# Optimization experiments

Hardware: AMD Instinct MI355X
Metric: run time of the kernel (lower is better)

The kernel has to match this reference:

```python
import jax, jax.numpy as jnp
import numpy as np

B, T, D, N = 64, 32, 128, 128


def setup_inputs() -> dict:
    key = jax.random.key(0)
    ks = jax.random.split(key, 7)
    init_mu = 0.05
    ini_sigma = -4.6
    inp = {
        'x': jax.random.normal(ks[0], (B, T, D), dtype=jnp.float32),
        'U_z': init_mu * jax.random.normal(ks[1], (D, N), dtype=jnp.float32),
        'W_z': init_mu * jax.random.normal(ks[2], (N, N), dtype=jnp.float32),
        'U_r': init_mu * jax.random.normal(ks[3], (D, N), dtype=jnp.float32),
        'W_r': init_mu * jax.random.normal(ks[4], (N, N), dtype=jnp.float32),
        'U_h': init_mu * jax.random.normal(ks[5], (D, N), dtype=jnp.float32),
        'W_h': init_mu * jax.random.normal(ks[6], (N, N), dtype=jnp.float32),
        'uz_sigma': jnp.full((N,), ini_sigma, dtype=jnp.float32),
        'wz_sigma': jnp.full((N,), ini_sigma, dtype=jnp.float32),
        'ur_sigma': jnp.full((N,), ini_sigma, dtype=jnp.float32),
        'wr_sigma': jnp.full((N,), ini_sigma, dtype=jnp.float32),
        'uh_sigma': jnp.full((N,), ini_sigma, dtype=jnp.float32),
        'wh_sigma': jnp.full((N,), ini_sigma, dtype=jnp.float32),
    }
    return inp


def _outer(a, b):
    # [B,n] x [B,n] -> [B,n,n]
    return a[:, :, None] * b[:, None, :]


def _hadamard_sigma(s1, s2, m1, m2):
    # s1*s2 + diag(m1) s2 diag(m1) + diag(m2) s1 diag(m2)
    return s1 * s2 + _outer(m1, m1) * s2 + _outer(m2, m2) * s1


def reference(x, U_z, W_z, U_r, W_r, U_h, W_h,
              uz_sigma, wz_sigma, ur_sigma, wr_sigma, uh_sigma, wh_sigma):
    b, t, d = x.shape
    n = U_z.shape[1]
    idx = jnp.arange(n)
    sp = jax.nn.softplus
    dUz, dWz = jnp.diag(sp(uz_sigma)), jnp.diag(sp(wz_sigma))
    dUr, dWr = jnp.diag(sp(ur_sigma)), jnp.diag(sp(wr_sigma))
    dUh, dWh = jnp.diag(sp(uh_sigma)), jnp.diag(sp(wh_sigma))

    def step(carry, xt):
        mu_p, S_p = carry  # [B,n], [B,n,n]
        xx = jnp.sum(xt * xt, axis=1)[:, None, None]
        pp = jnp.sum(mu_p * mu_p, axis=1)[:, None, None]
        trS = jnp.trace(S_p, axis1=1, axis2=2)[:, None, None]

        def gate_cov(W, dW, dU):
            # W^T Sigma W + ||prev||^2 dW + tr(Sigma) dW + ||x||^2 dU
            S1 = jnp.einsum('ki,bkl,lj->bij', W, S_p, W)
            return S1 + pp * dW + trS * dW + xx * dU

        az = xt @ U_z + mu_p @ W_z
        z = jax.nn.sigmoid(az)
        gz = z * (1.0 - z)
        S_z = gate_cov(W_z, dWz, dUz) * _outer(gz, gz)

        ar = xt @ U_r + mu_p @ W_r
        r = jax.nn.sigmoid(ar)
        gr = r * (1.0 - r)
        S_r = gate_cov(W_r, dWr, dUr) * _outer(gr, gr)

        rh = mu_p * r
        ah = xt @ U_h + rh @ W_h
        h = jnp.tanh(ah)
        gh = 1.0 - h * h
        S_g = _hadamard_sigma(S_p, S_r, mu_p, r)
        rr = jnp.sum(rh * rh, axis=1)[:, None, None]
        trg = jnp.trace(S_g, axis1=1, axis2=2)[:, None, None]
        S_hh = jnp.einsum('ki,bkl,lj->bij', W_h, S_g, W_h) + rr * dWh + trg * dWh + xx * dUh
        S_h = S_hh * _outer(gh, gh)

        mu = z * mu_p + (1.0 - z) * h
        sa = _hadamard_sigma(S_z, S_p, z, mu_p)
        sb = _hadamard_sigma(S_z, S_h, 1.0 - z, h)
        S = sa + sb - S_z * _outer(mu_p, h) - S_z * _outer(h, mu_p)
        S = jnp.where(jnp.isfinite(S), S, jnp.zeros_like(S))
        S = S.at[:, idx, idx].set(jnp.abs(S[:, idx, idx]))
        return (mu, S), (mu, S)

    mu0 = jnp.zeros((b, n), dtype=x.dtype)
    S0 = jnp.zeros((b, n, n), dtype=x.dtype)
    _, (mu_seq, S_seq) = jax.lax.scan(step, (mu0, S0), jnp.swapaxes(x, 0, 1))
    # [B,T,n], [B,T,n,n]
    return jnp.swapaxes(mu_seq, 0, 1), jnp.swapaxes(S_seq, 0, 1)
```

## Files before the change

kernel.cpp:

```cpp
#include <hip/hip_runtime.h>
#include <math.h>

#define B_ 64
#define T_ 32
#define D_ 128
#define N_ 128
#define SBS 72
#define PTS 136

typedef __attribute__((ext_vector_type(8))) short s8v;
typedef __attribute__((ext_vector_type(4))) float f4;

__device__ __forceinline__ float softplus_f(float v){ return (v > 20.f) ? v : log1pf(expf(v)); }
__device__ __forceinline__ float sigmoid_f(float v){ return 1.f / (1.f + expf(-v)); }
__device__ __forceinline__ float wred(float v){
#pragma unroll
    for (int o = 32; o > 0; o >>= 1) v += __shfl_down(v, o, 64);
    return v;
}
__device__ __forceinline__ void split2(float v, unsigned short& h, unsigned short& l){
    unsigned int u  = __float_as_uint(v);
    unsigned int rh = u + 0x7fffu + ((u >> 16) & 1u);
    h = (unsigned short)(rh >> 16);
    float fh = __uint_as_float(rh & 0xffff0000u);
    float lo = v - fh;
    unsigned int ul = __float_as_uint(lo);
    unsigned int rl = ul + 0x7fffu + ((ul >> 16) & 1u);
    l = (unsigned short)(rl >> 16);
}
__device__ __forceinline__ void split4_store(float4 v, unsigned short* hp, unsigned short* lp){
    unsigned short h0,h1,h2,h3,l0,l1,l2,l3;
    split2(v.x,h0,l0); split2(v.y,h1,l1); split2(v.z,h2,l2); split2(v.w,h3,l3);
    uint2 H = make_uint2((unsigned)h0 | ((unsigned)h1 << 16), (unsigned)h2 | ((unsigned)h3 << 16));
    uint2 L = make_uint2((unsigned)l0 | ((unsigned)l1 << 16), (unsigned)l2 | ((unsigned)l3 << 16));
    *(uint2*)hp = H; *(uint2*)lp = L;
}
__device__ __forceinline__ f4 mfma3(s8v ah, s8v al, s8v bh, s8v bl, f4 c){
    c = __builtin_amdgcn_mfma_f32_16x16x32_bf16(ah, bh, c, 0, 0, 0);
    c = __builtin_amdgcn_mfma_f32_16x16x32_bf16(ah, bl, c, 0, 0, 0);
    c = __builtin_amdgcn_mfma_f32_16x16x32_bf16(al, bh, c, 0, 0, 0);
    return c;
}

__global__ __launch_bounds__(256)
void prep_w(const float* __restrict__ Wz, const float* __restrict__ Wr,
            const float* __restrict__ Wh, unsigned short* __restrict__ WT){
    int gate = blockIdx.x, n0 = blockIdx.y * 16, tid = threadIdx.x;
    const float* W = (gate == 0) ? Wz : (gate == 1) ? Wr : Wh;
    unsigned short* hi = WT + (size_t)gate * 32768;
    unsigned short* lo = hi + 16384;
#pragma unroll
    for (int e = 0; e < 8; ++e){
        int idx = tid + e * 256;
        int n = n0 + (idx >> 7), k = idx & 127;
        float v = W[(size_t)k * 128 + n];
        unsigned short h, l; split2(v, h, l);
        hi[(size_t)n * 128 + k] = h;
        lo[(size_t)n * 128 + k] = l;
    }
}

__global__ __launch_bounds__(256)
void prep_xu(const float* __restrict__ x, const float* __restrict__ Uz,
             const float* __restrict__ Ur, const float* __restrict__ Uh,
             float* __restrict__ XU, float* __restrict__ XX){
    int bt = blockIdx.x, tid = threadIdx.x;
    __shared__ float sX[128];
    __shared__ float sRed[256];
    __shared__ float sP[4];
    if (tid < 128) sX[tid] = x[(size_t)bt * 128 + tid];
    __syncthreads();
    {
        float v = (tid < 128) ? sX[tid] * sX[tid] : 0.f;
        v = wred(v);
        if ((tid & 63) == 0) sP[tid >> 6] = v;
    }
    const float* Us[3] = {Uz, Ur, Uh};
#pragma unroll 1
    for (int g = 0; g < 3; ++g){
        int n = tid & 127, hf = tid >> 7;
        float p = 0.f;
#pragma unroll 8
        for (int k = hf * 64; k < hf * 64 + 64; ++k) p = fmaf(sX[k], Us[g][(size_t)k * 128 + n], p);
        sRed[tid] = p;
        __syncthreads();
        if (tid < 128) XU[(size_t)g * (2048 * 128) + (size_t)bt * 128 + tid] = sRed[tid] + sRed[tid + 128];
        __syncthreads();
    }
    if (tid == 0) XX[bt] = sP[0] + sP[1] + sP[2] + sP[3];
}

__global__ __launch_bounds__(256, 1)
void step_zr(const float* __restrict__ Wz, const float* __restrict__ Wr, const float* __restrict__ Wh,
             const float* __restrict__ uzs, const float* __restrict__ wzs,
             const float* __restrict__ urs, const float* __restrict__ wrs,
             const unsigned short* __restrict__ WT,
             const float* __restrict__ XU, const float* __restrict__ XX,
             float* __restrict__ mu_out, const float* __restrict__ S_out,
             float* __restrict__ wsSz, float* __restrict__ wsSr,
             float* __restrict__ wsVec, int t)
{
    const int b = blockIdx.y, j0 = blockIdx.x * 32, tid = threadIdx.x;
    const int lane = tid & 63, w = tid >> 6, q = (tid >> 4) & 3, lm = tid & 15;

    __shared__ alignas(16) char sBig[36864];
    unsigned short* sShi = (unsigned short*)sBig;
    unsigned short* sSlo = (unsigned short*)(sBig + 128 * SBS * 2);
    unsigned short* sPT  = (unsigned short*)sBig;

    __shared__ float sMu[128], sZ[128], sGz[128], sR[128], sGr[128], sRh[128];
    __shared__ float sSP[4][128];
    __shared__ float sRed[256];
    __shared__ float sScalA[4], sScalB[4], sScalC[4];

    const int bt = b * T_ + t;
    const float* Sp = (t > 0) ? (S_out + (size_t)(bt - 1) * 16384) : S_out;

    if (tid < 128) sMu[tid] = (t > 0) ? mu_out[(size_t)(bt - 1) * 128 + tid] : 0.f;
    for (int a = tid; a < 512; a += 256){
        int tb = a >> 7, n = a & 127;
        const float* src = (tb == 0) ? uzs : (tb == 1) ? wzs : (tb == 2) ? urs : wrs;
        sSP[tb][n] = softplus_f(src[n]);
    }
    __syncthreads();

    {
        int g = tid >> 7, n = tid & 127;
        const float* Wg = g ? Wr : Wz;
        float a = XU[(size_t)g * (2048 * 128) + (size_t)bt * 128 + n];
#pragma unroll 16
        for (int k = 0; k < 128; ++k) a = fmaf(sMu[k], Wg[(size_t)k * 128 + n], a);
        float gg = sigmoid_f(a);
        if (!g){ sZ[n] = gg; sGz[n] = gg * (1.f - gg); }
        else   { sR[n] = gg; sGr[n] = gg * (1.f - gg); }
    }
    __syncthreads();

    if (tid < 128) sRh[tid] = sMu[tid] * sR[tid];
    {
        float v1 = (tid < 128) ? sMu[tid] * sMu[tid] : 0.f;
        float v2 = (tid < 128 && t > 0) ? Sp[(size_t)tid * 129] : 0.f;
        v1 = wred(v1); v2 = wred(v2);
        if (lane == 0){ sScalA[w] = v1; sScalB[w] = v2; }
    }
    __syncthreads();

    {
        int n = tid & 127, hf = tid >> 7;
        float p = 0.f;
#pragma unroll 16
        for (int k = hf * 64; k < hf * 64 + 64; ++k) p = fmaf(sRh[k], Wh[(size_t)k * 128 + n], p);
        sRed[tid] = p;
        float v = (tid < 128) ? sRh[tid] * sRh[tid] : 0.f;
        v = wred(v);
        if (lane == 0) sScalC[w] = v;
    }
    __syncthreads();

    if (tid < 128){
        float ah = XU[(size_t)2 * (2048 * 128) + (size_t)bt * 128 + tid] + sRed[tid] + sRed[tid + 128];
        float h = tanhf(ah);
        float z = sZ[tid];
        if (blockIdx.x == 0){
            mu_out[(size_t)bt * 128 + tid] = z * sMu[tid] + (1.f - z) * h;
            float* vbp = wsVec + (size_t)b * 520;
            vbp[tid] = z; vbp[128 + tid] = sR[tid]; vbp[256 + tid] = h; vbp[384 + tid] = 1.f - h * h;
            if (tid == 0) vbp[512] = sScalC[0] + sScalC[1] + sScalC[2] + sScalC[3];
        }
    }

    f4 accP[8];
#pragma unroll
    for (int i = 0; i < 8; ++i) accP[i] = (f4){0.f, 0.f, 0.f, 0.f};

    for (int half = 0; half < 2; ++half){
        __syncthreads();
        {
            int l0g = half * 64;
#pragma unroll
            for (int i = 0; i < 8; ++i){
                int idx4 = tid + i * 256;
                int row = idx4 >> 4, c4 = idx4 & 15;
                float4 v = make_float4(0.f, 0.f, 0.f, 0.f);
                if (t > 0) v = *(const float4*)(Sp + (size_t)row * 128 + l0g + c4 * 4);
                split4_store(v, &sShi[row * SBS + c4 * 4], &sSlo[row * SBS + c4 * 4]);
            }
        }
        __syncthreads();
#pragma unroll
        for (int c = 0; c < 2; ++c){
            int lloc = c * 32 + q * 8;
            int lglob = half * 64 + lloc;
            s8v aH[2], aL[2];
#pragma unroll
            for (int s = 0; s < 2; ++s){
                int row = (w * 2 + s) * 16 + lm;
                aH[s] = *(const s8v*)&sShi[row * SBS + lloc];
                aL[s] = *(const s8v*)&sSlo[row * SBS + lloc];
            }
#pragma unroll
            for (int nt = 0; nt < 2; ++nt){
                size_t off = (size_t)(j0 + nt * 16 + lm) * 128 + lglob;
                s8v bzH = *(const s8v*)&WT[off];
                s8v bzL = *(const s8v*)&WT[16384 + off];
                s8v brH = *(const s8v*)&WT[32768 + off];
                s8v brL = *(const s8v*)&WT[49152 + off];
#pragma unroll
                for (int s = 0; s < 2; ++s){
                    accP[s * 2 + nt]     = mfma3(aH[s], aL[s], bzH, bzL, accP[s * 2 + nt]);
                    accP[4 + s * 2 + nt] = mfma3(aH[s], aL[s], brH, brL, accP[4 + s * 2 + nt]);
                }
            }
        }
    }
    __syncthreads();

#pragma unroll
    for (int g = 0; g < 2; ++g)
#pragma unroll
        for (int s = 0; s < 2; ++s)
#pragma unroll
            for (int nt = 0; nt < 2; ++nt){
                f4 a = accP[g * 4 + s * 2 + nt];
                int kb = (w * 2 + s) * 16 + q * 4;
                int jr = nt * 16 + lm;
                split4_store(make_float4(a[0], a[1], a[2], a[3]),
                             &sPT[(g * 2 + 0) * (32 * PTS) + jr * PTS + kb],
                             &sPT[(g * 2 + 1) * (32 * PTS) + jr * PTS + kb]);
            }
    __syncthreads();

    float pp  = sScalA[0] + sScalA[1] + sScalA[2] + sScalA[3];
    float trS = sScalB[0] + sScalB[1] + sScalB[2] + sScalB[3];
    float pt  = pp + trS;
    float xxv = XX[bt];

#pragma unroll 1
    for (int g = 0; g < 2; ++g){
        const unsigned short* AH = WT + (size_t)g * 32768;
        const unsigned short* AL = AH + 16384;
        const unsigned short* PH = sPT + (g * 2) * (32 * PTS);
        const unsigned short* PL = PH + (32 * PTS);
        f4 acc[4];
#pragma unroll
        for (int i = 0; i < 4; ++i) acc[i] = (f4){0.f, 0.f, 0.f, 0.f};
#pragma unroll
        for (int c = 0; c < 4; ++c){
            int k0 = c * 32 + q * 8;
            s8v aH[2], aL[2];
#pragma unroll
            for (int s = 0; s < 2; ++s){
                size_t row = (size_t)((w * 2 + s) * 16 + lm) * 128 + k0;
                aH[s] = *(const s8v*)&AH[row];
                aL[s] = *(const s8v*)&AL[row];
            }
#pragma unroll
            for (int nt = 0; nt < 2; ++nt){
                int jj = (nt * 16 + lm) * PTS + k0;
                s8v bH = *(const s8v*)&PH[jj];
                s8v bL = *(const s8v*)&PL[jj];
#pragma unroll
                for (int s = 0; s < 2; ++s)
                    acc[s * 2 + nt] = mfma3(aH[s], aL[s], bH, bL, acc[s * 2 + nt]);
            }
        }
        const float* G   = g ? sGr : sGz;
        const float* spU = g ? sSP[2] : sSP[0];
        const float* spW = g ? sSP[3] : sSP[1];
        float* dst = (g ? wsSr : wsSz) + (size_t)b * 16384;
#pragma unroll
        for (int s = 0; s < 2; ++s)
#pragma unroll
            for (int nt = 0; nt < 2; ++nt){
                f4 a = acc[s * 2 + nt];
                int ib = (w * 2 + s) * 16 + q * 4;
                int j = j0 + nt * 16 + lm;
                float gj = G[j];
#pragma unroll
                for (int r = 0; r < 4; ++r){
                    int i = ib + r;
                    float v = a[r];
                    if (i == j) v += pt * spW[i] + xxv * spU[i];
                    dst[(size_t)i * 128 + j] = v * G[i] * gj;
                }
            }
    }
}

__global__ __launch_bounds__(256, 1)
void step_h(const float* __restrict__ uhs, const float* __restrict__ whs,
            const unsigned short* __restrict__ WT,
            const float* __restrict__ XX,
            const float* __restrict__ mu_out, float* __restrict__ S_out,
            const float* __restrict__ wsSz, const float* __restrict__ wsSr,
            const float* __restrict__ wsVec, int t)
{
    const int b = blockIdx.y, j0 = blockIdx.x * 32, tid = threadIdx.x;
    const int lane = tid & 63, w = tid >> 6, q = (tid >> 4) & 3, lm = tid & 15;

    __shared__ alignas(16) char sBig[36864];
    unsigned short* sGhi = (unsigned short*)sBig;
    unsigned short* sGlo = (unsigned short*)(sBig + 128 * SBS * 2);
    unsigned short* sPT  = (unsigned short*)sBig;

    __shared__ float sMu[128], sZ[128], sR[128], sH[128], sGh[128];
    __shared__ float sSPu[128], sSPw[128];
    __shared__ float sScal[4];

    const int bt = b * T_ + t;
    const float* Sp = (t > 0) ? (S_out + (size_t)(bt - 1) * 16384) : S_out;
    const float* Sr = wsSr + (size_t)b * 16384;
    const float* vb = wsVec + (size_t)b * 520;
    const unsigned short* WTH = WT + 65536;
    const unsigned short* WTL = WT + 81920;

    if (tid < 128){
        sZ[tid] = vb[tid]; sR[tid] = vb[128 + tid]; sH[tid] = vb[256 + tid]; sGh[tid] = vb[384 + tid];
        sMu[tid] = (t > 0) ? mu_out[(size_t)(bt - 1) * 128 + tid] : 0.f;
        sSPu[tid] = softplus_f(uhs[tid]); sSPw[tid] = softplus_f(whs[tid]);
    }

    f4 accP[4];
#pragma unroll
    for (int i = 0; i < 4; ++i) accP[i] = (f4){0.f, 0.f, 0.f, 0.f};
    float tdiag = 0.f;

    for (int half = 0; half < 2; ++half){
        __syncthreads();
        {
            int l0g = half * 64;
#pragma unroll
            for (int i = 0; i < 8; ++i){
                int idx4 = tid + i * 256;
                int row = idx4 >> 4, c4 = idx4 & 15;
                int colg = l0g + c4 * 4;
                float4 sp4 = make_float4(0.f, 0.f, 0.f, 0.f);
                if (t > 0) sp4 = *(const float4*)(Sp + (size_t)row * 128 + colg);
                float4 sr4 = *(const float4*)(Sr + (size_t)row * 128 + colg);
                float muk = sMu[row], rk = sR[row];
                float4 mc = *(const float4*)&sMu[colg];
                float4 rc = *(const float4*)&sR[colg];
                float4 gv;
                gv.x = sp4.x * sr4.x + muk * mc.x * sr4.x + rk * rc.x * sp4.x;
                gv.y = sp4.y * sr4.y + muk * mc.y * sr4.y + rk * rc.y * sp4.y;
                gv.z = sp4.z * sr4.z + muk * mc.z * sr4.z + rk * rc.z * sp4.z;
                gv.w = sp4.w * sr4.w + muk * mc.w * sr4.w + rk * rc.w * sp4.w;
                int d = row - colg;
                if (d >= 0 && d < 4) tdiag += (d == 0) ? gv.x : (d == 1) ? gv.y : (d == 2) ? gv.z : gv.w;
                split4_store(gv, &sGhi[row * SBS + c4 * 4], &sGlo[row * SBS + c4 * 4]);
            }
        }
        __syncthreads();
#pragma unroll
        for (int c = 0; c < 2; ++c){
            int lloc = c * 32 + q * 8;
            int lglob = half * 64 + lloc;
            s8v aH[2], aL[2];
#pragma unroll
            for (int s = 0; s < 2; ++s){
                int row = (w * 2 + s) * 16 + lm;
                aH[s] = *(const s8v*)&sGhi[row * SBS + lloc];
                aL[s] = *(const s8v*)&sGlo[row * SBS + lloc];
            }
#pragma unroll
            for (int nt = 0; nt < 2; ++nt){
                size_t off = (size_t)(j0 + nt * 16 + lm) * 128 + lglob;
                s8v bH = *(const s8v*)&WTH[off];
                s8v bL = *(const s8v*)&WTL[off];
#pragma unroll
                for (int s = 0; s < 2; ++s)
                    accP[s * 2 + nt] = mfma3(aH[s], aL[s], bH, bL, accP[s * 2 + nt]);
            }
        }
    }
    float td = wred(tdiag);
    __syncthreads();
    if (lane == 0) sScal[w] = td;
#pragma unroll
    for (int s = 0; s < 2; ++s)
#pragma unroll
        for (int nt = 0; nt < 2; ++nt){
            f4 a = accP[s * 2 + nt];
            int kb = (w * 2 + s) * 16 + q * 4;
            int jr = nt * 16 + lm;
            split4_store(make_float4(a[0], a[1], a[2], a[3]),
                         &sPT[jr * PTS + kb],
                         &sPT[(32 * PTS) + jr * PTS + kb]);
        }
    __syncthreads();

    f4 acc[4];
#pragma unroll
    for (int i = 0; i < 4; ++i) acc[i] = (f4){0.f, 0.f, 0.f, 0.f};
#pragma unroll
    for (int c = 0; c < 4; ++c){
        int k0 = c * 32 + q * 8;
        s8v aH[2], aL[2];
#pragma unroll
        for (int s = 0; s < 2; ++s){
            size_t row = (size_t)((w * 2 + s) * 16 + lm) * 128 + k0;
            aH[s] = *(const s8v*)&WTH[row];
            aL[s] = *(const s8v*)&WTL[row];
        }
#pragma unroll
        for (int nt = 0; nt < 2; ++nt){
            int jj = (nt * 16 + lm) * PTS + k0;
            s8v bH = *(const s8v*)&sPT[jj];
            s8v bL = *(const s8v*)&sPT[(32 * PTS) + jj];
#pragma unroll
            for (int s = 0; s < 2; ++s)
                acc[s * 2 + nt] = mfma3(aH[s], aL[s], bH, bL, acc[s * 2 + nt]);
        }
    }

    float trg  = sScal[0] + sScal[1] + sScal[2] + sScal[3];
    float coef = vb[512] + trg;
    float xxv  = XX[bt];
    const float* Szb = wsSz + (size_t)b * 16384;
    float* outS = S_out + (size_t)bt * 16384;
#pragma unroll
    for (int s = 0; s < 2; ++s)
#pragma unroll
        for (int nt = 0; nt < 2; ++nt){
            f4 a = acc[s * 2 + nt];
            int ib = (w * 2 + s) * 16 + q * 4;
            int j = j0 + nt * 16 + lm;
            float zj = sZ[j], ghj = sGh[j];
#pragma unroll
            for (int r = 0; r < 4; ++r){
                int i = ib + r;
                float shh = a[r];
                if (i == j) shh += coef * sSPw[i] + xxv * sSPu[i];
                float sh = shh * sGh[i] * ghj;
                float szv = Szb[(size_t)i * 128 + j];
                float spv = (t > 0) ? Sp[(size_t)i * 128 + j] : 0.f;
                float dmi = sMu[i] - sH[i], dmj = sMu[j] - sH[j];
                float zi = sZ[i];
                float sv = szv * (spv + sh + dmi * dmj) + zi * zj * spv + (1.f - zi) * (1.f - zj) * sh;
                if (!isfinite(sv)) sv = 0.f;
                if (i == j) sv = fabsf(sv);
                outS[(size_t)i * 128 + j] = sv;
            }
        }
}

extern "C" void kernel_launch(void* const* d_in, const int* in_sizes, int n_in,
                              void* d_out, int out_size, void* d_ws, size_t ws_size,
                              hipStream_t stream)
{
    (void)in_sizes; (void)n_in; (void)out_size; (void)ws_size;
    const float* x   = (const float*)d_in[0];
    const float* Uz  = (const float*)d_in[1];
    const float* Wz  = (const float*)d_in[2];
    const float* Ur  = (const float*)d_in[3];
    const float* Wr  = (const float*)d_in[4];
    const float* Uh  = (const float*)d_in[5];
    const float* Wh  = (const float*)d_in[6];
    const float* uzs = (const float*)d_in[7];
    const float* wzs = (const float*)d_in[8];
    const float* urs = (const float*)d_in[9];
    const float* wrs = (const float*)d_in[10];
    const float* uhs = (const float*)d_in[11];
    const float* whs = (const float*)d_in[12];

    float* mu_out = (float*)d_out;
    float* S_out  = (float*)d_out + (size_t)B_ * T_ * N_;

    char* ws = (char*)d_ws;
    unsigned short* wsWT = (unsigned short*)ws;
    float* wsXU  = (float*)(ws + 196608);
    float* wsXX  = (float*)(ws + 3342336);
    float* wsSz  = (float*)(ws + 3350528);
    float* wsSr  = (float*)(ws + 7544832);
    float* wsVec = (float*)(ws + 11739136);

    hipLaunchKernelGGL(prep_w, dim3(3, 8), dim3(256), 0, stream, Wz, Wr, Wh, wsWT);
    hipLaunchKernelGGL(prep_xu, dim3(2048), dim3(256), 0, stream, x, Uz, Ur, Uh, wsXU, wsXX);

    dim3 grid(4, B_), blk(256);
    for (int t = 0; t < T_; ++t){
        hipLaunchKernelGGL(step_zr, grid, blk, 0, stream,
                           Wz, Wr, Wh, uzs, wzs, urs, wrs,
                           wsWT, wsXU, wsXX, mu_out, S_out, wsSz, wsSr, wsVec, t);
        hipLaunchKernelGGL(step_h, grid, blk, 0, stream,
                           uhs, whs, wsWT, wsXX, mu_out, S_out, wsSz, wsSr, wsVec, t);
    }
}
```

Measured before the change: 1.681 ms.

## Replace per-step kernel pairs with a persistent per-batch kernel keeping covariance in LDS

The 64 per-timestep launches (step_zr + step_h) are replaced by one persistent kernel with one 1024-thread block per batch element that loops over all 32 timesteps. The previous covariance stays resident in shared memory as split bf16 hi/lo, so it is no longer re-read from global memory, and the Sz/Sr intermediates stay in registers instead of going through workspace buffers. This removes launch overhead and global round-trips. The cost is that only 64 blocks run on the device, so per-step parallelism and occupancy drop, and shared-memory pressure is high.

```diff
diff --git a/kernel.cpp b/kernel.cpp
--- a/kernel.cpp
+++ b/kernel.cpp
@@ -3,10 +3,8 @@
 
 #define B_ 64
 #define T_ 32
-#define D_ 128
 #define N_ 128
-#define SBS 72
-#define PTS 136
+#define SST 136
 
 typedef __attribute__((ext_vector_type(8))) short s8v;
 typedef __attribute__((ext_vector_type(4))) float f4;
@@ -34,6 +32,9 @@
     uint2 H = make_uint2((unsigned)h0 | ((unsigned)h1 << 16), (unsigned)h2 | ((unsigned)h3 << 16));
     uint2 L = make_uint2((unsigned)l0 | ((unsigned)l1 << 16), (unsigned)l2 | ((unsigned)l3 << 16));
     *(uint2*)hp = H; *(uint2*)lp = L;
+}
+__device__ __forceinline__ float rec16(unsigned short h, unsigned short l){
+    return __uint_as_float((unsigned)h << 16) + __uint_as_float((unsigned)l << 16);
 }
 __device__ __forceinline__ f4 mfma3(s8v ah, s8v al, s8v bh, s8v bl, f4 c){
     c = __builtin_amdgcn_mfma_f32_16x16x32_bf16(ah, bh, c, 0, 0, 0);
@@ -90,358 +91,260 @@
     if (tid == 0) XX[bt] = sP[0] + sP[1] + sP[2] + sP[3];
 }
 
-__global__ __launch_bounds__(256, 1)
-void step_zr(const float* __restrict__ Wz, const float* __restrict__ Wr, const float* __restrict__ Wh,
-             const float* __restrict__ uzs, const float* __restrict__ wzs,
-             const float* __restrict__ urs, const float* __restrict__ wrs,
-             const unsigned short* __restrict__ WT,
-             const float* __restrict__ XU, const float* __restrict__ XX,
-             float* __restrict__ mu_out, const float* __restrict__ S_out,
-             float* __restrict__ wsSz, float* __restrict__ wsSr,
-             float* __restrict__ wsVec, int t)
-{
-    const int b = blockIdx.y, j0 = blockIdx.x * 32, tid = threadIdx.x;
-    const int lane = tid & 63, w = tid >> 6, q = (tid >> 4) & 3, lm = tid & 15;
-
-    __shared__ alignas(16) char sBig[36864];
-    unsigned short* sShi = (unsigned short*)sBig;
-    unsigned short* sSlo = (unsigned short*)(sBig + 128 * SBS * 2);
-    unsigned short* sPT  = (unsigned short*)sBig;
-
-    __shared__ float sMu[128], sZ[128], sGz[128], sR[128], sGr[128], sRh[128];
-    __shared__ float sSP[4][128];
-    __shared__ float sRed[256];
-    __shared__ float sScalA[4], sScalB[4], sScalC[4];
-
-    const int bt = b * T_ + t;
-    const float* Sp = (t > 0) ? (S_out + (size_t)(bt - 1) * 16384) : S_out;
-
-    if (tid < 128) sMu[tid] = (t > 0) ? mu_out[(size_t)(bt - 1) * 128 + tid] : 0.f;
-    for (int a = tid; a < 512; a += 256){
-        int tb = a >> 7, n = a & 127;
-        const float* src = (tb == 0) ? uzs : (tb == 1) ? wzs : (tb == 2) ? urs : wrs;
-        sSP[tb][n] = softplus_f(src[n]);
-    }
-    __syncthreads();
-
-    {
-        int g = tid >> 7, n = tid & 127;
-        const float* Wg = g ? Wr : Wz;
-        float a = XU[(size_t)g * (2048 * 128) + (size_t)bt * 128 + n];
-#pragma unroll 16
-        for (int k = 0; k < 128; ++k) a = fmaf(sMu[k], Wg[(size_t)k * 128 + n], a);
-        float gg = sigmoid_f(a);
-        if (!g){ sZ[n] = gg; sGz[n] = gg * (1.f - gg); }
-        else   { sR[n] = gg; sGr[n] = gg * (1.f - gg); }
-    }
-    __syncthreads();
-
-    if (tid < 128) sRh[tid] = sMu[tid] * sR[tid];
-    {
-        float v1 = (tid < 128) ? sMu[tid] * sMu[tid] : 0.f;
-        float v2 = (tid < 128 && t > 0) ? Sp[(size_t)tid * 129] : 0.f;
-        v1 = wred(v1); v2 = wred(v2);
-        if (lane == 0){ sScalA[w] = v1; sScalB[w] = v2; }
-    }
-    __syncthreads();
-
-    {
-        int n = tid & 127, hf = tid >> 7;
-        float p = 0.f;
-#pragma unroll 16
-        for (int k = hf * 64; k < hf * 64 + 64; ++k) p = fmaf(sRh[k], Wh[(size_t)k * 128 + n], p);
-        sRed[tid] = p;
-        float v = (tid < 128) ? sRh[tid] * sRh[tid] : 0.f;
-        v = wred(v);
-        if (lane == 0) sScalC[w] = v;
-    }
-    __syncthreads();
-
-    if (tid < 128){
-        float ah = XU[(size_t)2 * (2048 * 128) + (size_t)bt * 128 + tid] + sRed[tid] + sRed[tid + 128];
-        float h = tanhf(ah);
-        float z = sZ[tid];
-        if (blockIdx.x == 0){
-            mu_out[(size_t)bt * 128 + tid] = z * sMu[tid] + (1.f - z) * h;
-            float* vbp = wsVec + (size_t)b * 520;
-            vbp[tid] = z; vbp[128 + tid] = sR[tid]; vbp[256 + tid] = h; vbp[384 + tid] = 1.f - h * h;
-            if (tid == 0) vbp[512] = sScalC[0] + sScalC[1] + sScalC[2] + sScalC[3];
-        }
-    }
-
-    f4 accP[8];
-#pragma unroll
-    for (int i = 0; i < 8; ++i) accP[i] = (f4){0.f, 0.f, 0.f, 0.f};
-
-    for (int half = 0; half < 2; ++half){
-        __syncthreads();
-        {
-            int l0g = half * 64;
-#pragma unroll
-            for (int i = 0; i < 8; ++i){
-                int idx4 = tid + i * 256;
-                int row = idx4 >> 4, c4 = idx4 & 15;
-                float4 v = make_float4(0.f, 0.f, 0.f, 0.f);
-                if (t > 0) v = *(const float4*)(Sp + (size_t)row * 128 + l0g + c4 * 4);
-                split4_store(v, &sShi[row * SBS + c4 * 4], &sSlo[row * SBS + c4 * 4]);
-            }
-        }
-        __syncthreads();
-#pragma unroll
-        for (int c = 0; c < 2; ++c){
-            int lloc = c * 32 + q * 8;
-            int lglob = half * 64 + lloc;
-            s8v aH[2], aL[2];
-#pragma unroll
-            for (int s = 0; s < 2; ++s){
-                int row = (w * 2 + s) * 16 + lm;
-                aH[s] = *(const s8v*)&sShi[row * SBS + lloc];
-                aL[s] = *(const s8v*)&sSlo[row * SBS + lloc];
-            }
-#pragma unroll
-            for (int nt = 0; nt < 2; ++nt){
-                size_t off = (size_t)(j0 + nt * 16 + lm) * 128 + lglob;
-                s8v bzH = *(const s8v*)&WT[off];
-                s8v bzL = *(const s8v*)&WT[16384 + off];
-                s8v brH = *(const s8v*)&WT[32768 + off];
-                s8v brL = *(const s8v*)&WT[49152 + off];
-#pragma unroll
-                for (int s = 0; s < 2; ++s){
-                    accP[s * 2 + nt]     = mfma3(aH[s], aL[s], bzH, bzL, accP[s * 2 + nt]);
-                    accP[4 + s * 2 + nt] = mfma3(aH[s], aL[s], brH, brL, accP[4 + s * 2 + nt]);
-                }
-            }
-        }
-    }
-    __syncthreads();
-
-#pragma unroll
-    for (int g = 0; g < 2; ++g)
-#pragma unroll
-        for (int s = 0; s < 2; ++s)
-#pragma unroll
-            for (int nt = 0; nt < 2; ++nt){
-                f4 a = accP[g * 4 + s * 2 + nt];
-                int kb = (w * 2 + s) * 16 + q * 4;
-                int jr = nt * 16 + lm;
-                split4_store(make_float4(a[0], a[1], a[2], a[3]),
-                             &sPT[(g * 2 + 0) * (32 * PTS) + jr * PTS + kb],
-                             &sPT[(g * 2 + 1) * (32 * PTS) + jr * PTS + kb]);
-            }
-    __syncthreads();
-
-    float pp  = sScalA[0] + sScalA[1] + sScalA[2] + sScalA[3];
-    float trS = sScalB[0] + sScalB[1] + sScalB[2] + sScalB[3];
-    float pt  = pp + trS;
-    float xxv = XX[bt];
-
-#pragma unroll 1
-    for (int g = 0; g < 2; ++g){
-        const unsigned short* AH = WT + (size_t)g * 32768;
-        const unsigned short* AL = AH + 16384;
-        const unsigned short* PH = sPT + (g * 2) * (32 * PTS);
-        const unsigned short* PL = PH + (32 * PTS);
-        f4 acc[4];
-#pragma unroll
-        for (int i = 0; i < 4; ++i) acc[i] = (f4){0.f, 0.f, 0.f, 0.f};
-#pragma unroll
-        for (int c = 0; c < 4; ++c){
-            int k0 = c * 32 + q * 8;
-            s8v aH[2], aL[2];
-#pragma unroll
-            for (int s = 0; s < 2; ++s){
-                size_t row = (size_t)((w * 2 + s) * 16 + lm) * 128 + k0;
-                aH[s] = *(const s8v*)&AH[row];
-                aL[s] = *(const s8v*)&AL[row];
-            }
-#pragma unroll
-            for (int nt = 0; nt < 2; ++nt){
-                int jj = (nt * 16 + lm) * PTS + k0;
-                s8v bH = *(const s8v*)&PH[jj];
-                s8v bL = *(const s8v*)&PL[jj];
-#pragma unroll
-                for (int s = 0; s < 2; ++s)
-                    acc[s * 2 + nt] = mfma3(aH[s], aL[s], bH, bL, acc[s * 2 + nt]);
-            }
-        }
-        const float* G   = g ? sGr : sGz;
-        const float* spU = g ? sSP[2] : sSP[0];
-        const float* spW = g ? sSP[3] : sSP[1];
-        float* dst = (g ? wsSr : wsSz) + (size_t)b * 16384;
-#pragma unroll
-        for (int s = 0; s < 2; ++s)
-#pragma unroll
-            for (int nt = 0; nt < 2; ++nt){
-                f4 a = acc[s * 2 + nt];
-                int ib = (w * 2 + s) * 16 + q * 4;
-                int j = j0 + nt * 16 + lm;
-                float gj = G[j];
-#pragma unroll
-                for (int r = 0; r < 4; ++r){
-                    int i = ib + r;
-                    float v = a[r];
-                    if (i == j) v += pt * spW[i] + xxv * spU[i];
-                    dst[(size_t)i * 128 + j] = v * G[i] * gj;
-                }
-            }
-    }
-}
-
-__global__ __launch_bounds__(256, 1)
-void step_h(const float* __restrict__ uhs, const float* __restrict__ whs,
-            const unsigned short* __restrict__ WT,
-            const float* __restrict__ XX,
-            const float* __restrict__ mu_out, float* __restrict__ S_out,
-            const float* __restrict__ wsSz, const float* __restrict__ wsSr,
-            const float* __restrict__ wsVec, int t)
-{
-    const int b = blockIdx.y, j0 = blockIdx.x * 32, tid = threadIdx.x;
-    const int lane = tid & 63, w = tid >> 6, q = (tid >> 4) & 3, lm = tid & 15;
-
-    __shared__ alignas(16) char sBig[36864];
-    unsigned short* sGhi = (unsigned short*)sBig;
-    unsigned short* sGlo = (unsigned short*)(sBig + 128 * SBS * 2);
-    unsigned short* sPT  = (unsigned short*)sBig;
-
-    __shared__ float sMu[128], sZ[128], sR[128], sH[128], sGh[128];
-    __shared__ float sSPu[128], sSPw[128];
-    __shared__ float sScal[4];
-
-    const int bt = b * T_ + t;
-    const float* Sp = (t > 0) ? (S_out + (size_t)(bt - 1) * 16384) : S_out;
-    const float* Sr = wsSr + (size_t)b * 16384;
-    const float* vb = wsVec + (size_t)b * 520;
-    const unsigned short* WTH = WT + 65536;
-    const unsigned short* WTL = WT + 81920;
-
-    if (tid < 128){
-        sZ[tid] = vb[tid]; sR[tid] = vb[128 + tid]; sH[tid] = vb[256 + tid]; sGh[tid] = vb[384 + tid];
-        sMu[tid] = (t > 0) ? mu_out[(size_t)(bt - 1) * 128 + tid] : 0.f;
-        sSPu[tid] = softplus_f(uhs[tid]); sSPw[tid] = softplus_f(whs[tid]);
-    }
-
-    f4 accP[4];
-#pragma unroll
-    for (int i = 0; i < 4; ++i) accP[i] = (f4){0.f, 0.f, 0.f, 0.f};
-    float tdiag = 0.f;
-
-    for (int half = 0; half < 2; ++half){
-        __syncthreads();
-        {
-            int l0g = half * 64;
-#pragma unroll
-            for (int i = 0; i < 8; ++i){
-                int idx4 = tid + i * 256;
-                int row = idx4 >> 4, c4 = idx4 & 15;
-                int colg = l0g + c4 * 4;
-                float4 sp4 = make_float4(0.f, 0.f, 0.f, 0.f);
-                if (t > 0) sp4 = *(const float4*)(Sp + (size_t)row * 128 + colg);
-                float4 sr4 = *(const float4*)(Sr + (size_t)row * 128 + colg);
-                float muk = sMu[row], rk = sR[row];
-                float4 mc = *(const float4*)&sMu[colg];
-                float4 rc = *(const float4*)&sR[colg];
-                float4 gv;
-                gv.x = sp4.x * sr4.x + muk * mc.x * sr4.x + rk * rc.x * sp4.x;
-                gv.y = sp4.y * sr4.y + muk * mc.y * sr4.y + rk * rc.y * sp4.y;
-                gv.z = sp4.z * sr4.z + muk * mc.z * sr4.z + rk * rc.z * sp4.z;
-                gv.w = sp4.w * sr4.w + muk * mc.w * sr4.w + rk * rc.w * sp4.w;
-                int d = row - colg;
-                if (d >= 0 && d < 4) tdiag += (d == 0) ? gv.x : (d == 1) ? gv.y : (d == 2) ? gv.z : gv.w;
-                split4_store(gv, &sGhi[row * SBS + c4 * 4], &sGlo[row * SBS + c4 * 4]);
-            }
-        }
-        __syncthreads();
-#pragma unroll
-        for (int c = 0; c < 2; ++c){
-            int lloc = c * 32 + q * 8;
-            int lglob = half * 64 + lloc;
-            s8v aH[2], aL[2];
-#pragma unroll
-            for (int s = 0; s < 2; ++s){
-                int row = (w * 2 + s) * 16 + lm;
-                aH[s] = *(const s8v*)&sGhi[row * SBS + lloc];
-                aL[s] = *(const s8v*)&sGlo[row * SBS + lloc];
-            }
-#pragma unroll
-            for (int nt = 0; nt < 2; ++nt){
-                size_t off = (size_t)(j0 + nt * 16 + lm) * 128 + lglob;
-                s8v bH = *(const s8v*)&WTH[off];
-                s8v bL = *(const s8v*)&WTL[off];
-#pragma unroll
-                for (int s = 0; s < 2; ++s)
-                    accP[s * 2 + nt] = mfma3(aH[s], aL[s], bH, bL, accP[s * 2 + nt]);
-            }
-        }
-    }
-    float td = wred(tdiag);
-    __syncthreads();
-    if (lane == 0) sScal[w] = td;
-#pragma unroll
-    for (int s = 0; s < 2; ++s)
-#pragma unroll
-        for (int nt = 0; nt < 2; ++nt){
-            f4 a = accP[s * 2 + nt];
-            int kb = (w * 2 + s) * 16 + q * 4;
-            int jr = nt * 16 + lm;
-            split4_store(make_float4(a[0], a[1], a[2], a[3]),
-                         &sPT[jr * PTS + kb],
-                         &sPT[(32 * PTS) + jr * PTS + kb]);
-        }
-    __syncthreads();
-
-    f4 acc[4];
-#pragma unroll
-    for (int i = 0; i < 4; ++i) acc[i] = (f4){0.f, 0.f, 0.f, 0.f};
+__device__ __forceinline__ void mm1_run(const unsigned short* AH, const unsigned short* AL,
+                                        const unsigned short* BW, f4* accP,
+                                        int r16, int c64, int q, int lm)
+{
 #pragma unroll
     for (int c = 0; c < 4; ++c){
         int k0 = c * 32 + q * 8;
-        s8v aH[2], aL[2];
-#pragma unroll
-        for (int s = 0; s < 2; ++s){
-            size_t row = (size_t)((w * 2 + s) * 16 + lm) * 128 + k0;
-            aH[s] = *(const s8v*)&WTH[row];
-            aL[s] = *(const s8v*)&WTL[row];
-        }
-#pragma unroll
-        for (int nt = 0; nt < 2; ++nt){
-            int jj = (nt * 16 + lm) * PTS + k0;
-            s8v bH = *(const s8v*)&sPT[jj];
-            s8v bL = *(const s8v*)&sPT[(32 * PTS) + jj];
-#pragma unroll
-            for (int s = 0; s < 2; ++s)
-                acc[s * 2 + nt] = mfma3(aH[s], aL[s], bH, bL, acc[s * 2 + nt]);
-        }
-    }
-
-    float trg  = sScal[0] + sScal[1] + sScal[2] + sScal[3];
-    float coef = vb[512] + trg;
-    float xxv  = XX[bt];
-    const float* Szb = wsSz + (size_t)b * 16384;
-    float* outS = S_out + (size_t)bt * 16384;
-#pragma unroll
-    for (int s = 0; s < 2; ++s)
-#pragma unroll
-        for (int nt = 0; nt < 2; ++nt){
-            f4 a = acc[s * 2 + nt];
-            int ib = (w * 2 + s) * 16 + q * 4;
-            int j = j0 + nt * 16 + lm;
-            float zj = sZ[j], ghj = sGh[j];
+        s8v aH = *(const s8v*)&AH[(r16 * 16 + lm) * SST + k0];
+        s8v aL = *(const s8v*)&AL[(r16 * 16 + lm) * SST + k0];
+#pragma unroll
+        for (int nt = 0; nt < 4; ++nt){
+            int j = c64 * 64 + nt * 16 + lm;
+            s8v bH = *(const s8v*)&BW[j * 128 + k0];
+            s8v bL = *(const s8v*)&BW[16384 + j * 128 + k0];
+            accP[nt] = mfma3(aH, aL, bH, bL, accP[nt]);
+        }
+    }
+}
+__device__ __forceinline__ void pt_write(const f4* accP, unsigned short* PTh, unsigned short* PTl,
+                                         int r16, int c64, int q, int lm)
+{
+#pragma unroll
+    for (int nt = 0; nt < 4; ++nt){
+        f4 a = accP[nt];
+        int j = c64 * 64 + nt * 16 + lm;
+        int k = r16 * 16 + q * 4;
+        split4_store(make_float4(a[0], a[1], a[2], a[3]), &PTh[j * SST + k], &PTl[j * SST + k]);
+    }
+}
+__device__ __forceinline__ void mm2_run(const unsigned short* WA, const unsigned short* PTh,
+                                        const unsigned short* PTl, f4* acc2,
+                                        int c16, int r64, int q, int lm)
+{
+#pragma unroll
+    for (int c = 0; c < 4; ++c){
+        int k0 = c * 32 + q * 8;
+        s8v bH = *(const s8v*)&PTh[(c16 * 16 + lm) * SST + k0];
+        s8v bL = *(const s8v*)&PTl[(c16 * 16 + lm) * SST + k0];
+#pragma unroll
+        for (int s = 0; s < 4; ++s){
+            int i = r64 * 64 + s * 16 + lm;
+            s8v aH = *(const s8v*)&WA[i * 128 + k0];
+            s8v aL = *(const s8v*)&WA[16384 + i * 128 + k0];
+            acc2[s] = mfma3(aH, aL, bH, bL, acc2[s]);
+        }
+    }
+}
+
+__global__ __launch_bounds__(1024, 4)
+void gru_persist(const float* __restrict__ Wz, const float* __restrict__ Wr,
+                 const float* __restrict__ Wh,
+                 const float* __restrict__ uzs, const float* __restrict__ wzs,
+                 const float* __restrict__ urs, const float* __restrict__ wrs,
+                 const float* __restrict__ uhs, const float* __restrict__ whs,
+                 const unsigned short* __restrict__ WT,
+                 const float* __restrict__ XU, const float* __restrict__ XX,
+                 float* __restrict__ mu_out, float* __restrict__ S_out)
+{
+    const int b = blockIdx.x, tid = threadIdx.x;
+    const int lane = tid & 63, w = tid >> 6, q = (tid >> 4) & 3, lm = tid & 15;
+    const int r16 = w & 7, c64 = w >> 3;
+    const int c16 = w & 7, r64 = w >> 3;
+
+    __shared__ unsigned short sPhi[128 * SST];
+    __shared__ unsigned short sPlo[128 * SST];
+    __shared__ unsigned short sR2[2 * 128 * SST];
+    __shared__ float sMu[128], sMuN[128], sZ[128], sGz[128], sR[128], sGr[128],
+                     sRh[128], sH[128], sGh[128];
+    __shared__ float sSP[6][128];
+    __shared__ float sRed[1024];
+    __shared__ float sScal[8];
+
+    unsigned short* PTh = sR2;
+    unsigned short* PTl = sR2 + 128 * SST;
+    const unsigned short* WTz = WT;
+    const unsigned short* WTr = WT + 32768;
+    const unsigned short* WTh = WT + 65536;
+
+    for (int i = tid; i < 128 * SST; i += 1024){ sPhi[i] = 0; sPlo[i] = 0; }
+    if (tid < 128) sMu[tid] = 0.f;
+    if (tid < 768){
+        int tb = tid >> 7, n = tid & 127;
+        const float* src = (tb == 0) ? uzs : (tb == 1) ? wzs : (tb == 2) ? urs :
+                           (tb == 3) ? wrs : (tb == 4) ? uhs : whs;
+        sSP[tb][n] = softplus_f(src[n]);
+    }
+    __syncthreads();
+
+    float szv[4][4];
+    float sgv[4][4];
+
+#pragma unroll 1
+    for (int t = 0; t < T_; ++t){
+        const int bt = b * T_ + t;
+
+        if (tid < 128){
+            float mu = sMu[tid];
+            float v1 = mu * mu;
+            float v2 = rec16(sPhi[tid * SST + tid], sPlo[tid * SST + tid]);
+            v1 = wred(v1); v2 = wred(v2);
+            if (lane == 0){ sScal[w * 2] = v1; sScal[w * 2 + 1] = v2; }
+        }
+        {
+            int g = tid >> 9, n = tid & 127, seg = (tid >> 7) & 3;
+            const float* Wg = g ? Wr : Wz;
+            float p = 0.f;
+#pragma unroll
+            for (int k = seg * 32; k < seg * 32 + 32; ++k) p = fmaf(sMu[k], Wg[k * N_ + n], p);
+            sRed[tid] = p;
+        }
+        __syncthreads();
+        if (tid < 256){
+            int g = tid >> 7, n = tid & 127;
+            float a = XU[(size_t)g * 262144 + (size_t)bt * 128 + n];
+            a += sRed[g * 512 + n] + sRed[g * 512 + 128 + n]
+               + sRed[g * 512 + 256 + n] + sRed[g * 512 + 384 + n];
+            float gg = sigmoid_f(a);
+            if (!g){ sZ[n] = gg; sGz[n] = gg * (1.f - gg); }
+            else   { sR[n] = gg; sGr[n] = gg * (1.f - gg); }
+        }
+        __syncthreads();
+        if (tid < 128){
+            float rh = sMu[tid] * sR[tid]; sRh[tid] = rh;
+            float v = rh * rh; v = wred(v);
+            if (lane == 0) sScal[4 + w] = v;
+        }
+        __syncthreads();
+        {
+            int n = tid & 127, seg = tid >> 7;
+            float p = 0.f;
+#pragma unroll
+            for (int k = seg * 16; k < seg * 16 + 16; ++k) p = fmaf(sRh[k], Wh[k * N_ + n], p);
+            sRed[tid] = p;
+        }
+        __syncthreads();
+        if (tid < 128){
+            float a = XU[(size_t)2 * 262144 + (size_t)bt * 128 + tid];
+#pragma unroll
+            for (int s = 0; s < 8; ++s) a += sRed[s * 128 + tid];
+            float h = tanhf(a);
+            sH[tid] = h; sGh[tid] = 1.f - h * h;
+            float z = sZ[tid];
+            float mun = z * sMu[tid] + (1.f - z) * h;
+            sMuN[tid] = mun;
+            mu_out[(size_t)bt * 128 + tid] = mun;
+        }
+        __syncthreads();
+
+        const float xx = XX[bt];
+        const float pt = sScal[0] + sScal[2] + sScal[1] + sScal[3];
+        const float rr = sScal[4] + sScal[5];
+
+        f4 accP[4], acc2[4];
+#pragma unroll
+        for (int i = 0; i < 4; ++i) accP[i] = (f4){0.f, 0.f, 0.f, 0.f};
+        mm1_run(sPhi, sPlo, WTz, accP, r16, c64, q, lm);
+        pt_write(accP, PTh, PTl, r16, c64, q, lm);
+        __syncthreads();
+#pragma unroll
+        for (int i = 0; i < 4; ++i) acc2[i] = (f4){0.f, 0.f, 0.f, 0.f};
+        mm2_run(WTz, PTh, PTl, acc2, c16, r64, q, lm);
+#pragma unroll
+        for (int s = 0; s < 4; ++s)
 #pragma unroll
             for (int r = 0; r < 4; ++r){
-                int i = ib + r;
-                float shh = a[r];
-                if (i == j) shh += coef * sSPw[i] + xxv * sSPu[i];
-                float sh = shh * sGh[i] * ghj;
-                float szv = Szb[(size_t)i * 128 + j];
-                float spv = (t > 0) ? Sp[(size_t)i * 128 + j] : 0.f;
+                int i = r64 * 64 + s * 16 + q * 4 + r;
+                int j = c16 * 16 + lm;
+                float v = acc2[s][r];
+                if (i == j) v += pt * sSP[1][i] + xx * sSP[0][i];
+                szv[s][r] = v * sGz[i] * sGz[j];
+            }
+
+#pragma unroll
+        for (int i = 0; i < 4; ++i) accP[i] = (f4){0.f, 0.f, 0.f, 0.f};
+        mm1_run(sPhi, sPlo, WTr, accP, r16, c64, q, lm);
+        __syncthreads();
+        pt_write(accP, PTh, PTl, r16, c64, q, lm);
+        __syncthreads();
+#pragma unroll
+        for (int i = 0; i < 4; ++i) acc2[i] = (f4){0.f, 0.f, 0.f, 0.f};
+        mm2_run(WTr, PTh, PTl, acc2, c16, r64, q, lm);
+        float tdiag = 0.f;
+#pragma unroll
+        for (int s = 0; s < 4; ++s)
+#pragma unroll
+            for (int r = 0; r < 4; ++r){
+                int i = r64 * 64 + s * 16 + q * 4 + r;
+                int j = c16 * 16 + lm;
+                float v = acc2[s][r];
+                if (i == j) v += pt * sSP[3][i] + xx * sSP[2][i];
+                float sr = v * sGr[i] * sGr[j];
+                float sp = rec16(sPhi[i * SST + j], sPlo[i * SST + j]);
+                float sg = sr * (sp + sMu[i] * sMu[j]) + sR[i] * sR[j] * sp;
+                if (i == j) tdiag += sg;
+                sgv[s][r] = sg;
+            }
+        __syncthreads();
+#pragma unroll
+        for (int s = 0; s < 4; ++s)
+#pragma unroll
+            for (int r = 0; r < 4; ++r){
+                int i = r64 * 64 + s * 16 + q * 4 + r;
+                int j = c16 * 16 + lm;
+                unsigned short hh, ll; split2(sgv[s][r], hh, ll);
+                PTh[i * SST + j] = hh;
+                PTl[i * SST + j] = ll;
+            }
+        {
+            float td = wred(tdiag);
+            if (lane == 0) sRed[w] = td;
+        }
+        __syncthreads();
+
+#pragma unroll
+        for (int i = 0; i < 4; ++i) accP[i] = (f4){0.f, 0.f, 0.f, 0.f};
+        mm1_run(PTh, PTl, WTh, accP, r16, c64, q, lm);
+        __syncthreads();
+        pt_write(accP, PTh, PTl, r16, c64, q, lm);
+        __syncthreads();
+#pragma unroll
+        for (int i = 0; i < 4; ++i) acc2[i] = (f4){0.f, 0.f, 0.f, 0.f};
+        mm2_run(WTh, PTh, PTl, acc2, c16, r64, q, lm);
+
+        float trg = 0.f;
+#pragma unroll
+        for (int i = 0; i < 16; ++i) trg += sRed[i];
+        const float coef = rr + trg;
+        float* outS = S_out + (size_t)bt * 16384;
+#pragma unroll
+        for (int s = 0; s < 4; ++s)
+#pragma unroll
+            for (int r = 0; r < 4; ++r){
+                int i = r64 * 64 + s * 16 + q * 4 + r;
+                int j = c16 * 16 + lm;
+                float shh = acc2[s][r];
+                if (i == j) shh += coef * sSP[5][i] + xx * sSP[4][i];
+                float sh = shh * sGh[i] * sGh[j];
+                float sp = rec16(sPhi[i * SST + j], sPlo[i * SST + j]);
+                float sz = szv[s][r];
                 float dmi = sMu[i] - sH[i], dmj = sMu[j] - sH[j];
-                float zi = sZ[i];
-                float sv = szv * (spv + sh + dmi * dmj) + zi * zj * spv + (1.f - zi) * (1.f - zj) * sh;
+                float zi = sZ[i], zj = sZ[j];
+                float sv = sz * (sp + sh + dmi * dmj) + zi * zj * sp
+                         + (1.f - zi) * (1.f - zj) * sh;
                 if (!isfinite(sv)) sv = 0.f;
                 if (i == j) sv = fabsf(sv);
                 outS[(size_t)i * 128 + j] = sv;
+                unsigned short hh, ll; split2(sv, hh, ll);
+                sPhi[i * SST + j] = hh;
+                sPlo[i * SST + j] = ll;
             }
-        }
+        __syncthreads();
+        if (tid < 128) sMu[tid] = sMuN[tid];
+        __syncthreads();
+    }
 }
 
 extern "C" void kernel_launch(void* const* d_in, const int* in_sizes, int n_in,
@@ -468,21 +371,12 @@
 
     char* ws = (char*)d_ws;
     unsigned short* wsWT = (unsigned short*)ws;
-    float* wsXU  = (float*)(ws + 196608);
-    float* wsXX  = (float*)(ws + 3342336);
-    float* wsSz  = (float*)(ws + 3350528);
-    float* wsSr  = (float*)(ws + 7544832);
-    float* wsVec = (float*)(ws + 11739136);
+    float* wsXU = (float*)(ws + 196608);
+    float* wsXX = (float*)(ws + 3342336);
 
     hipLaunchKernelGGL(prep_w, dim3(3, 8), dim3(256), 0, stream, Wz, Wr, Wh, wsWT);
     hipLaunchKernelGGL(prep_xu, dim3(2048), dim3(256), 0, stream, x, Uz, Ur, Uh, wsXU, wsXX);
-
-    dim3 grid(4, B_), blk(256);
-    for (int t = 0; t < T_; ++t){
-        hipLaunchKernelGGL(step_zr, grid, blk, 0, stream,
-                           Wz, Wr, Wh, uzs, wzs, urs, wrs,
-                           wsWT, wsXU, wsXX, mu_out, S_out, wsSz, wsSr, wsVec, t);
-        hipLaunchKernelGGL(step_h, grid, blk, 0, stream,
-                           uhs, whs, wsWT, wsXX, mu_out, S_out, wsSz, wsSr, wsVec, t);
-    }
-}
+    hipLaunchKernelGGL(gru_persist, dim3(B_), dim3(1024), 0, stream,
+                       Wz, Wr, Wh, uzs, wzs, urs, wrs, uhs, whs,
+                       wsWT, wsXU, wsXX, mu_out, S_out);
+}
```

Result: slower. 4.284 ms (+154.8%).
